# Kernel optimization log

Hardware: AMD Instinct MI355X
Metric: run time of the kernel (lower is better)

## Reference

```python
import jax, jax.numpy as jnp
import numpy as np

LOG2PI = float(np.log(2.0 * np.pi))
T, S, D, K = 1024, 512, 32, 64


def setup_inputs() -> dict:
    key = jax.random.key(0)
    k0, k1, k2, k3, k4 = jax.random.split(key, 5)
    data = jax.random.normal(k0, (T, S, D), dtype=jnp.float32)  # packed time-major
    ip = jax.random.uniform(k1, (K,), dtype=jnp.float32)
    initial_probs = ip / ip.sum()
    A = jax.random.uniform(k2, (K, K), dtype=jnp.float32)
    transition_probs = A / A.sum(-1, keepdims=True)  # row-stochastic
    means = jax.random.normal(k3, (K, D), dtype=jnp.float32)
    covars = jax.random.uniform(k4, (K, D), dtype=jnp.float32) * 0.5 + 0.5  # positive diag
    return {"data": data, "initial_probs": initial_probs,
            "transition_probs": transition_probs, "means": means, "covars": covars}


def _emission_probs(data, means, covars):
    # Gaussian diag-covariance densities, [T, S, K], without materializing [T,S,K,D].
    inv = 1.0 / covars  # [K, D]
    quad = (jnp.einsum('tsd,kd->tsk', data * data, inv)
            - 2.0 * jnp.einsum('tsd,kd->tsk', data, means * inv)
            + (means * means * inv).sum(-1))  # [T, S, K]
    logp = -0.5 * (quad + jnp.log(covars).sum(-1) + data.shape[-1] * LOG2PI)
    return jnp.exp(logp)


def reference(data, initial_probs, transition_probs, means, covars):
    probs = _emission_probs(data, means, covars)  # [T, S, K]
    # t = 0: alpha = normalize(initial * emission)
    a0 = initial_probs * probs[0]
    d0 = a0.sum(-1, keepdims=True)
    alpha0 = a0 / d0
    log_denom0 = jnp.log(d0)  # [S, 1]

    def step(carry, p_t):
        alpha, log_denom = carry
        a = p_t * (alpha @ transition_probs)  # [S, K]
        d = a.sum(-1, keepdims=True)
        return (a / d, log_denom + jnp.log(d)), None

    (alpha, log_denom), _ = jax.lax.scan(step, (alpha0, log_denom0), probs[1:])
    log_likeli = jax.nn.logsumexp(jnp.log(alpha) + log_denom, axis=-1).sum()
    return alpha, -log_likeli
```

## Files before the change

### kernel.cpp

```cpp
#include <hip/hip_runtime.h>
#include <hip/hip_fp16.h>
#include <math.h>

#define TT 1024
#define SS 512
#define DD 32
#define KK 64

#define LOG2PI_F 1.8378770664093453f

#define NSEG 4
#define SEGLEN (TT / NSEG)
#define BURN 64

#define PBUF_BYTES ((size_t)TT * SS * KK * 2)
#define EM_WPB 4
#define EM_BLOCKS 2048
#define NWAVES (EM_BLOCKS * EM_WPB)

typedef float v2f __attribute__((ext_vector_type(2)));

__device__ __forceinline__ v2f fma2(v2f a, v2f b, v2f c) {
#if __has_builtin(__builtin_elementwise_fma)
    return __builtin_elementwise_fma(a, b, c);
#else
    v2f r; r.x = fmaf(a.x, b.x, c.x); r.y = fmaf(a.y, b.y, c.y); return r;
#endif
}

template <int CTRL, int RMASK>
__device__ __forceinline__ float dpp_add(float x) {
    int t = __builtin_amdgcn_update_dpp(0, __float_as_int(x), CTRL, RMASK, 0xf, true);
    return x + __int_as_float(t);
}
template <int CTRL, int RMASK>
__device__ __forceinline__ float dpp_max(float x) {
    int xi = __float_as_int(x);
    int t = __builtin_amdgcn_update_dpp(xi, xi, CTRL, RMASK, 0xf, false);
    return fmaxf(x, __int_as_float(t));
}
__device__ __forceinline__ float wave_reduce_sum(float x) {
    x = dpp_add<0x111, 0xf>(x);
    x = dpp_add<0x112, 0xf>(x);
    x = dpp_add<0x114, 0xf>(x);
    x = dpp_add<0x118, 0xf>(x);
    x = dpp_add<0x142, 0xa>(x);
    x = dpp_add<0x143, 0xc>(x);
    return __int_as_float(__builtin_amdgcn_readlane(__float_as_int(x), 63));
}
__device__ __forceinline__ float wave_reduce_max(float x) {
    x = dpp_max<0x111, 0xf>(x);
    x = dpp_max<0x112, 0xf>(x);
    x = dpp_max<0x114, 0xf>(x);
    x = dpp_max<0x118, 0xf>(x);
    x = dpp_max<0x142, 0xa>(x);
    x = dpp_max<0x143, 0xc>(x);
    return __int_as_float(__builtin_amdgcn_readlane(__float_as_int(x), 63));
}

__global__ __launch_bounds__(EM_WPB * 64)
__attribute__((amdgpu_waves_per_eu(1, 3)))
void emission_kernel(
    const float* __restrict__ data,
    const float* __restrict__ means,
    const float* __restrict__ covars,
    __half* __restrict__ pbuf,
    float* __restrict__ mpart)
{
    const int k  = threadIdx.x & 63;
    const int w  = threadIdx.x >> 6;
    const int wv = blockIdx.x * EM_WPB + w;

    v2f w2[DD / 2], m2[DD / 2];
    float c0 = DD * LOG2PI_F;
#pragma unroll
    for (int d = 0; d < DD; ++d) {
        float c = covars[k * DD + d];
        ((float*)w2)[d] = 1.0f / c;
        ((float*)m2)[d] = means[k * DD + d];
        c0 += __logf(c);
    }

    __shared__ __align__(16) float4 xst[EM_WPB][2][64];

    const int base = wv * 64;
    const float4* dsrc = (const float4*)(data + (size_t)base * DD);

    float4 xr = dsrc[k];
    xst[w][0][k] = xr;
    __builtin_amdgcn_wave_barrier();

    float macc = 0.0f;
    int cur = 0;

    for (int b = 0; b < 8; ++b) {
        const int bn = (b + 1 < 8) ? (b + 1) : 7;
        xr = dsrc[bn * 64 + k];

        const float* xb = (const float*)&xst[w][cur][0];
#pragma unroll
        for (int i = 0; i < 8; i += 2) {
            const float4* x0q = (const float4*)(xb + i * DD);
            const float4* x1q = (const float4*)(xb + (i + 1) * DD);
            v2f p00 = {0,0}, p01 = {0,0}, p10 = {0,0}, p11 = {0,0};
#pragma unroll
            for (int d4 = 0; d4 < DD / 8; ++d4) {
                float4 x0 = x0q[d4];
                float4 x1 = x1q[d4];
                v2f xa0; xa0.x = x0.x; xa0.y = x0.y;
                v2f xb0; xb0.x = x0.z; xb0.y = x0.w;
                v2f xa1; xa1.x = x1.x; xa1.y = x1.y;
                v2f xb1; xb1.x = x1.z; xb1.y = x1.w;
                v2f ta0 = xa0 - m2[2 * d4],     tb0 = xb0 - m2[2 * d4 + 1];
                v2f ta1 = xa1 - m2[2 * d4],     tb1 = xb1 - m2[2 * d4 + 1];
                p00 = fma2(w2[2 * d4] * ta0, ta0, p00);
                p01 = fma2(w2[2 * d4 + 1] * tb0, tb0, p01);
                p10 = fma2(w2[2 * d4] * ta1, ta1, p10);
                p11 = fma2(w2[2 * d4 + 1] * tb1, tb1, p11);
            }
#pragma unroll
            for (int d4 = DD / 8; d4 < DD / 4; ++d4) {
                float4 x0 = x0q[d4];
                float4 x1 = x1q[d4];
                v2f xa0; xa0.x = x0.x; xa0.y = x0.y;
                v2f xb0; xb0.x = x0.z; xb0.y = x0.w;
                v2f xa1; xa1.x = x1.x; xa1.y = x1.y;
                v2f xb1; xb1.x = x1.z; xb1.y = x1.w;
                v2f ta0 = xa0 - m2[2 * d4],     tb0 = xb0 - m2[2 * d4 + 1];
                v2f ta1 = xa1 - m2[2 * d4],     tb1 = xb1 - m2[2 * d4 + 1];
                p00 = fma2(w2[2 * d4] * ta0, ta0, p00);
                p01 = fma2(w2[2 * d4 + 1] * tb0, tb0, p01);
                p10 = fma2(w2[2 * d4] * ta1, ta1, p10);
                p11 = fma2(w2[2 * d4 + 1] * tb1, tb1, p11);
            }
            v2f s0 = p00 + p01, s1 = p10 + p11;
            float logp0 = -0.5f * ((s0.x + s0.y) + c0);
            float logp1 = -0.5f * ((s1.x + s1.y) + c0);
            float mx0 = wave_reduce_max(logp0);
            float mx1 = wave_reduce_max(logp1);
            const int item0 = base + b * 8 + i;
            pbuf[(size_t)item0 * KK + k]        = __float2half(__expf(logp0 - mx0));
            pbuf[(size_t)(item0 + 1) * KK + k]  = __float2half(__expf(logp1 - mx1));
            macc += mx0 + mx1;
        }

        xst[w][cur ^ 1][k] = xr;
        __builtin_amdgcn_wave_barrier();
        cur ^= 1;
    }
    if (k == 0) mpart[wv] = macc;
}

__global__ __launch_bounds__(64)
__attribute__((amdgpu_waves_per_eu(1, 2)))
void hmm_seq(
    const __half* __restrict__ pbuf,
    const float* __restrict__ initial,
    const float* __restrict__ trans,
    float* __restrict__ out_alpha,
    float* __restrict__ seq_logd)
{
    const int s   = blockIdx.x;
    const int seg = blockIdx.y;
    const int k   = threadIdx.x;

    const int emit_from = seg * SEGLEN;
    const int t0        = seg ? (emit_from - BURN) : 0;
    const int nsteps    = seg ? (SEGLEN + BURN) : SEGLEN;

    v2f acl[KK / 2];
#pragma unroll
    for (int j = 0; j < KK / 2; ++j) {
        acl[j].x = trans[(2 * j) * KK + k];
        acl[j].y = trans[(2 * j + 1) * KK + k];
    }

    __shared__ __align__(16) float alpha_sh[KK];

    const __half* pp = pbuf + (size_t)s * KK + k;
    const size_t PST = (size_t)SS * KK;

    __half pf[8];
#pragma unroll
    for (int i = 0; i < 8; ++i) pf[i] = pp[PST * (size_t)(t0 + i)];

    const float init_k = seg ? 1.0f : initial[k];
    float logd = 0.0f;
    float a = 0.0f;

    for (int mblk = 0; mblk < nsteps / 8; ++mblk) {
#pragma unroll
        for (int i = 0; i < 8; ++i) {
            const int t = t0 + 8 * mblk + i;
            const float pc = __half2float(pf[i]);
            int tn = t + 8; if (tn >= TT) tn = TT - 1;
            pf[i] = pp[PST * (size_t)tn];

            if (mblk == 0 && i == 0) {
                a = init_k * pc;
            } else {
                const float4* ash4 = (const float4*)alpha_sh;
                v2f a0 = {0,0}, a1 = {0,0}, a2 = {0,0}, a3 = {0,0};
#pragma unroll
                for (int j4 = 0; j4 < KK / 4; ++j4) {
                    float4 av = ash4[j4];
                    v2f lo; lo.x = av.x; lo.y = av.y;
                    v2f hi; hi.x = av.z; hi.y = av.w;
                    if (j4 & 1) {
                        a2 = fma2(lo, acl[2 * j4], a2);
                        a3 = fma2(hi, acl[2 * j4 + 1], a3);
                    } else {
                        a0 = fma2(lo, acl[2 * j4], a0);
                        a1 = fma2(hi, acl[2 * j4 + 1], a1);
                    }
                }
                v2f sv = (a0 + a1) + (a2 + a3);
                a = pc * (sv.x + sv.y);
            }

            if ((t & 3) == 3) {
                float den = wave_reduce_sum(a);
                logd += (t >= emit_from) ? __logf(den) : 0.0f;
                a *= __builtin_amdgcn_rcpf(den);
            }

            alpha_sh[k] = a;
            __builtin_amdgcn_wave_barrier();
        }
    }

    if (seg == NSEG - 1) out_alpha[(size_t)s * KK + k] = a;
    if (k == 0) seq_logd[seg * SS + s] = logd;
}

__global__ __launch_bounds__(256) void finalize(
    const float* __restrict__ seq_logd, const float* __restrict__ mpart,
    float* __restrict__ out_nll)
{
    float v = 0.0f;
    for (int j = threadIdx.x; j < NWAVES; j += 256) v += mpart[j];
    for (int j = threadIdx.x; j < NSEG * SS; j += 256) v += seq_logd[j];
#pragma unroll
    for (int off = 32; off > 0; off >>= 1)
        v += __shfl_xor(v, off, 64);
    __shared__ float sh[4];
    if ((threadIdx.x & 63) == 0) sh[threadIdx.x >> 6] = v;
    __syncthreads();
    if (threadIdx.x == 0) {
        double total = ((double)sh[0] + sh[1]) + ((double)sh[2] + sh[3]);
        out_nll[0] = (float)(-total);
    }
}

extern "C" void kernel_launch(void* const* d_in, const int* in_sizes, int n_in,
                              void* d_out, int out_size, void* d_ws, size_t ws_size,
                              hipStream_t stream) {
    const float* data    = (const float*)d_in[0];
    const float* initial = (const float*)d_in[1];
    const float* trans   = (const float*)d_in[2];
    const float* means   = (const float*)d_in[3];
    const float* covars  = (const float*)d_in[4];

    float* out_alpha = (float*)d_out;
    float* out_nll   = (float*)d_out + (size_t)SS * KK;

    __half* pbuf     = (__half*)d_ws;
    float*  mpart    = (float*)((char*)d_ws + PBUF_BYTES);
    float*  seq_logd = (float*)((char*)d_ws + PBUF_BYTES + NWAVES * sizeof(float));

    emission_kernel<<<EM_BLOCKS, EM_WPB * 64, 0, stream>>>(
        data, means, covars, pbuf, mpart);
    hmm_seq<<<dim3(SS, NSEG), 64, 0, stream>>>(
        pbuf, initial, trans, out_alpha, seq_logd);
    finalize<<<1, 256, 0, stream>>>(seq_logd, mpart, out_nll);
}
```

Baseline: 293.1 us.

## Batch 16 sequences per wave and run HMM forward recursion on MFMA

Replaces the per-sequence scalar forward recursion with a kernel in which each wave handles 16 sequences. It computes alpha@A as 16x16x32 fp16 MFMAs, with the transition matrix held in registers and emission tiles staged through double-buffered LDS. Normalization now runs every step using a 16-lane rowsum instead of every fourth step, and the time axis is split into 16 segments (with burn-in) instead of 4 for more parallelism. The alpha state is now rounded to fp16 between steps, which risks accuracy, and the burn-in overhead grows relative to the shorter segments.

```diff
diff --git a/kernel.cpp b/kernel.cpp
--- a/kernel.cpp
+++ b/kernel.cpp
@@ -9,7 +9,8 @@
 
 #define LOG2PI_F 1.8378770664093453f
 
-#define NSEG 4
+#define QSEQ 16
+#define NSEG 16
 #define SEGLEN (TT / NSEG)
 #define BURN 64
 
@@ -19,6 +20,8 @@
 #define NWAVES (EM_BLOCKS * EM_WPB)
 
 typedef float v2f __attribute__((ext_vector_type(2)));
+typedef float f32x4 __attribute__((ext_vector_type(4)));
+typedef _Float16 h8 __attribute__((ext_vector_type(8)));
 
 __device__ __forceinline__ v2f fma2(v2f a, v2f b, v2f c) {
 #if __has_builtin(__builtin_elementwise_fma)
@@ -29,24 +32,10 @@
 }
 
 template <int CTRL, int RMASK>
-__device__ __forceinline__ float dpp_add(float x) {
-    int t = __builtin_amdgcn_update_dpp(0, __float_as_int(x), CTRL, RMASK, 0xf, true);
-    return x + __int_as_float(t);
-}
-template <int CTRL, int RMASK>
 __device__ __forceinline__ float dpp_max(float x) {
     int xi = __float_as_int(x);
     int t = __builtin_amdgcn_update_dpp(xi, xi, CTRL, RMASK, 0xf, false);
     return fmaxf(x, __int_as_float(t));
-}
-__device__ __forceinline__ float wave_reduce_sum(float x) {
-    x = dpp_add<0x111, 0xf>(x);
-    x = dpp_add<0x112, 0xf>(x);
-    x = dpp_add<0x114, 0xf>(x);
-    x = dpp_add<0x118, 0xf>(x);
-    x = dpp_add<0x142, 0xa>(x);
-    x = dpp_add<0x143, 0xc>(x);
-    return __int_as_float(__builtin_amdgcn_readlane(__float_as_int(x), 63));
 }
 __device__ __forceinline__ float wave_reduce_max(float x) {
     x = dpp_max<0x111, 0xf>(x);
@@ -56,6 +45,19 @@
     x = dpp_max<0x142, 0xa>(x);
     x = dpp_max<0x143, 0xc>(x);
     return __int_as_float(__builtin_amdgcn_readlane(__float_as_int(x), 63));
+}
+template <int N>
+__device__ __forceinline__ float dpp_ror_add(float x) {
+    int xi = __float_as_int(x);
+    int t = __builtin_amdgcn_update_dpp(xi, xi, 0x120 + N, 0xf, 0xf, false);
+    return x + __int_as_float(t);
+}
+__device__ __forceinline__ float rowsum16(float x) {
+    x = dpp_ror_add<8>(x);
+    x = dpp_ror_add<4>(x);
+    x = dpp_ror_add<2>(x);
+    x = dpp_ror_add<1>(x);
+    return x;
 }
 
 __global__ __launch_bounds__(EM_WPB * 64)
@@ -104,30 +106,15 @@
             const float4* x1q = (const float4*)(xb + (i + 1) * DD);
             v2f p00 = {0,0}, p01 = {0,0}, p10 = {0,0}, p11 = {0,0};
 #pragma unroll
-            for (int d4 = 0; d4 < DD / 8; ++d4) {
+            for (int d4 = 0; d4 < DD / 4; ++d4) {
                 float4 x0 = x0q[d4];
                 float4 x1 = x1q[d4];
                 v2f xa0; xa0.x = x0.x; xa0.y = x0.y;
                 v2f xb0; xb0.x = x0.z; xb0.y = x0.w;
                 v2f xa1; xa1.x = x1.x; xa1.y = x1.y;
                 v2f xb1; xb1.x = x1.z; xb1.y = x1.w;
-                v2f ta0 = xa0 - m2[2 * d4],     tb0 = xb0 - m2[2 * d4 + 1];
-                v2f ta1 = xa1 - m2[2 * d4],     tb1 = xb1 - m2[2 * d4 + 1];
-                p00 = fma2(w2[2 * d4] * ta0, ta0, p00);
-                p01 = fma2(w2[2 * d4 + 1] * tb0, tb0, p01);
-                p10 = fma2(w2[2 * d4] * ta1, ta1, p10);
-                p11 = fma2(w2[2 * d4 + 1] * tb1, tb1, p11);
-            }
-#pragma unroll
-            for (int d4 = DD / 8; d4 < DD / 4; ++d4) {
-                float4 x0 = x0q[d4];
-                float4 x1 = x1q[d4];
-                v2f xa0; xa0.x = x0.x; xa0.y = x0.y;
-                v2f xb0; xb0.x = x0.z; xb0.y = x0.w;
-                v2f xa1; xa1.x = x1.x; xa1.y = x1.y;
-                v2f xb1; xb1.x = x1.z; xb1.y = x1.w;
-                v2f ta0 = xa0 - m2[2 * d4],     tb0 = xb0 - m2[2 * d4 + 1];
-                v2f ta1 = xa1 - m2[2 * d4],     tb1 = xb1 - m2[2 * d4 + 1];
+                v2f ta0 = xa0 - m2[2 * d4],  tb0 = xb0 - m2[2 * d4 + 1];
+                v2f ta1 = xa1 - m2[2 * d4],  tb1 = xb1 - m2[2 * d4 + 1];
                 p00 = fma2(w2[2 * d4] * ta0, ta0, p00);
                 p01 = fma2(w2[2 * d4 + 1] * tb0, tb0, p01);
                 p10 = fma2(w2[2 * d4] * ta1, ta1, p10);
@@ -139,8 +126,8 @@
             float mx0 = wave_reduce_max(logp0);
             float mx1 = wave_reduce_max(logp1);
             const int item0 = base + b * 8 + i;
-            pbuf[(size_t)item0 * KK + k]        = __float2half(__expf(logp0 - mx0));
-            pbuf[(size_t)(item0 + 1) * KK + k]  = __float2half(__expf(logp1 - mx1));
+            pbuf[(size_t)item0 * KK + k]       = __float2half(__expf(logp0 - mx0));
+            pbuf[(size_t)(item0 + 1) * KK + k] = __float2half(__expf(logp1 - mx1));
             macc += mx0 + mx1;
         }
 
@@ -151,86 +138,153 @@
     if (k == 0) mpart[wv] = macc;
 }
 
+#define RSTR 72
+
 __global__ __launch_bounds__(64)
-__attribute__((amdgpu_waves_per_eu(1, 2)))
-void hmm_seq(
+__attribute__((amdgpu_waves_per_eu(1, 1)))
+void hmm_mfma(
     const __half* __restrict__ pbuf,
     const float* __restrict__ initial,
     const float* __restrict__ trans,
     float* __restrict__ out_alpha,
     float* __restrict__ seq_logd)
 {
-    const int s   = blockIdx.x;
-    const int seg = blockIdx.y;
-    const int k   = threadIdx.x;
+    const int lane = threadIdx.x;
+    const int col  = lane & 15;
+    const int grp  = lane >> 4;
+    const int s0   = blockIdx.x * QSEQ;
+    const int seg  = blockIdx.y;
 
     const int emit_from = seg * SEGLEN;
     const int t0        = seg ? (emit_from - BURN) : 0;
     const int nsteps    = seg ? (SEGLEN + BURN) : SEGLEN;
 
-    v2f acl[KK / 2];
-#pragma unroll
-    for (int j = 0; j < KK / 2; ++j) {
-        acl[j].x = trans[(2 * j) * KK + k];
-        acl[j].y = trans[(2 * j + 1) * KK + k];
-    }
-
-    __shared__ __align__(16) float alpha_sh[KK];
-
-    const __half* pp = pbuf + (size_t)s * KK + k;
-    const size_t PST = (size_t)SS * KK;
-
-    __half pf[8];
-#pragma unroll
-    for (int i = 0; i < 8; ++i) pf[i] = pp[PST * (size_t)(t0 + i)];
-
-    const float init_k = seg ? 1.0f : initial[k];
-    float logd = 0.0f;
-    float a = 0.0f;
-
-    for (int mblk = 0; mblk < nsteps / 8; ++mblk) {
-#pragma unroll
-        for (int i = 0; i < 8; ++i) {
-            const int t = t0 + 8 * mblk + i;
-            const float pc = __half2float(pf[i]);
-            int tn = t + 8; if (tn >= TT) tn = TT - 1;
-            pf[i] = pp[PST * (size_t)tn];
-
-            if (mblk == 0 && i == 0) {
-                a = init_k * pc;
+    h8 bf[2][4];
+#pragma unroll
+    for (int kc = 0; kc < 2; ++kc)
+#pragma unroll
+        for (int nt = 0; nt < 4; ++nt) {
+            h8 v;
+#pragma unroll
+            for (int e = 0; e < 8; ++e) {
+                int j = kc * 32 + grp * 8 + e;
+                v[e] = (_Float16)trans[j * KK + nt * 16 + col];
+            }
+            bf[kc][nt] = v;
+        }
+
+    float init_c[4];
+#pragma unroll
+    for (int nt = 0; nt < 4; ++nt)
+        init_c[nt] = seg ? 1.0f : initial[nt * 16 + col];
+
+    __shared__ __align__(16) _Float16 ash[QSEQ * RSTR];
+    __shared__ __align__(16) _Float16 plds[2][4 * QSEQ * RSTR];
+
+    float4 pr[8];
+#define XLOAD(TB)                                                             \
+    {                                                                         \
+        const float4* src = (const float4*)(pbuf +                            \
+            (((size_t)((TB) + grp)) * SS + s0 + col) * KK);                   \
+        _Pragma("unroll")                                                     \
+        for (int e = 0; e < 8; ++e) pr[e] = src[e];                           \
+    }
+#define XWRITE(BUF)                                                           \
+    {                                                                         \
+        float4* dst = (float4*)(&plds[BUF][(grp * 16 + col) * RSTR]);         \
+        _Pragma("unroll")                                                     \
+        for (int e = 0; e < 8; ++e) dst[e] = pr[e];                           \
+    }
+
+    XLOAD(t0);
+    XWRITE(0);
+    __builtin_amdgcn_wave_barrier();
+
+    h8 a0, a1;
+    float ld[4] = {0.0f, 0.0f, 0.0f, 0.0f};
+    int cur = 0;
+
+    for (int g = 0; g < nsteps / 4; ++g) {
+        const int tbase = t0 + 4 * g;
+        int tb_next = tbase + 4;
+        if (tb_next > TT - 4) tb_next = TT - 4;
+        XLOAD(tb_next);
+
+        const _Float16* pc_base = &plds[cur][0];
+#pragma unroll
+        for (int st = 0; st < 4; ++st) {
+            const int t = tbase + st;
+            f32x4 c[4];
+            if (g == 0 && st == 0) {
+#pragma unroll
+                for (int nt = 0; nt < 4; ++nt) {
+                    f32x4 z = {init_c[nt], init_c[nt], init_c[nt], init_c[nt]};
+                    c[nt] = z;
+                }
             } else {
-                const float4* ash4 = (const float4*)alpha_sh;
-                v2f a0 = {0,0}, a1 = {0,0}, a2 = {0,0}, a3 = {0,0};
-#pragma unroll
-                for (int j4 = 0; j4 < KK / 4; ++j4) {
-                    float4 av = ash4[j4];
-                    v2f lo; lo.x = av.x; lo.y = av.y;
-                    v2f hi; hi.x = av.z; hi.y = av.w;
-                    if (j4 & 1) {
-                        a2 = fma2(lo, acl[2 * j4], a2);
-                        a3 = fma2(hi, acl[2 * j4 + 1], a3);
-                    } else {
-                        a0 = fma2(lo, acl[2 * j4], a0);
-                        a1 = fma2(hi, acl[2 * j4 + 1], a1);
-                    }
+                f32x4 z = {0.0f, 0.0f, 0.0f, 0.0f};
+#pragma unroll
+                for (int nt = 0; nt < 4; ++nt) {
+                    c[nt] = __builtin_amdgcn_mfma_f32_16x16x32_f16(
+                        a0, bf[0][nt], z, 0, 0, 0);
+                    c[nt] = __builtin_amdgcn_mfma_f32_16x16x32_f16(
+                        a1, bf[1][nt], c[nt], 0, 0, 0);
                 }
-                v2f sv = (a0 + a1) + (a2 + a3);
-                a = pc * (sv.x + sv.y);
             }
 
-            if ((t & 3) == 3) {
-                float den = wave_reduce_sum(a);
-                logd += (t >= emit_from) ? __logf(den) : 0.0f;
-                a *= __builtin_amdgcn_rcpf(den);
+            float av[4][4];
+            float pden[4] = {0.0f, 0.0f, 0.0f, 0.0f};
+#pragma unroll
+            for (int nt = 0; nt < 4; ++nt)
+#pragma unroll
+                for (int j = 0; j < 4; ++j) {
+                    float pcv = (float)pc_base[
+                        (st * 16 + grp * 4 + j) * RSTR + nt * 16 + col];
+                    float v = c[nt][j] * pcv;
+                    av[nt][j] = v;
+                    pden[j] += v;
+                }
+
+            float r[4];
+#pragma unroll
+            for (int j = 0; j < 4; ++j) {
+                float den = rowsum16(pden[j]);
+                if (t >= emit_from) ld[j] += __logf(den);
+                r[j] = __builtin_amdgcn_rcpf(den);
             }
 
-            alpha_sh[k] = a;
+#pragma unroll
+            for (int nt = 0; nt < 4; ++nt)
+#pragma unroll
+                for (int j = 0; j < 4; ++j)
+                    ash[(grp * 4 + j) * RSTR + nt * 16 + col] =
+                        (_Float16)(av[nt][j] * r[j]);
+            __builtin_amdgcn_wave_barrier();
+            a0 = *(const h8*)(ash + col * RSTR + grp * 8);
+            a1 = *(const h8*)(ash + col * RSTR + 32 + grp * 8);
             __builtin_amdgcn_wave_barrier();
         }
-    }
-
-    if (seg == NSEG - 1) out_alpha[(size_t)s * KK + k] = a;
-    if (k == 0) seq_logd[seg * SS + s] = logd;
+
+        XWRITE(cur ^ 1);
+        __builtin_amdgcn_wave_barrier();
+        cur ^= 1;
+    }
+#undef XLOAD
+#undef XWRITE
+
+    if (seg == NSEG - 1) {
+#pragma unroll
+        for (int nt = 0; nt < 4; ++nt)
+#pragma unroll
+            for (int j = 0; j < 4; ++j)
+                out_alpha[(size_t)(s0 + grp * 4 + j) * KK + nt * 16 + col] =
+                    (float)ash[(grp * 4 + j) * RSTR + nt * 16 + col];
+    }
+    if (col == 0) {
+#pragma unroll
+        for (int j = 0; j < 4; ++j)
+            seq_logd[seg * SS + s0 + grp * 4 + j] = ld[j];
+    }
 }
 
 __global__ __launch_bounds__(256) void finalize(
@@ -270,7 +324,7 @@
 
     emission_kernel<<<EM_BLOCKS, EM_WPB * 64, 0, stream>>>(
         data, means, covars, pbuf, mpart);
-    hmm_seq<<<dim3(SS, NSEG), 64, 0, stream>>>(
+    hmm_mfma<<<dim3(SS / QSEQ, NSEG), 64, 0, stream>>>(
         pbuf, initial, trans, out_alpha, seq_logd);
     finalize<<<1, 256, 0, stream>>>(seq_logd, mpart, out_nll);
 }
```

Measured after the change: 287.6 us. About the same (-1.9%).
